# Performance work log

Hardware: AMD Instinct MI355X
Metric: run time of the kernel (lower is better)

The kernel has to match this reference:

```python
import jax, jax.numpy as jnp
import numpy as np

B, N, D_MODEL, H = 2, 2048, 1024, 16
Q_CHUNK, K_CHUNK = 512, 1024
LN_EPS = 1e-5


def layer_norm(x, g, b):
    mu = x.mean(-1, keepdims=True)
    var = ((x - mu) ** 2).mean(-1, keepdims=True)
    return (x - mu) * jax.lax.rsqrt(var + LN_EPS) * g + b


def chunked_attention(q, k, v, qry_chunk, key_chunk):
    # q,k,v: [b,h,n,d]; memory-efficient chunked online-softmax attention
    b, h, n, d = q.shape
    q = q * (d ** -0.5)
    Q, K = n // qry_chunk, n // key_chunk
    qr = q.reshape(b, h, Q, qry_chunk, d)
    kr = k.reshape(b, h, K, key_chunk, d)
    vr = v.reshape(b, h, K, key_chunk, d)
    # per (q-chunk, k-chunk) scores: [b,h,Q,K,i,j]
    qk = jnp.einsum('bhqid,bhkjd->bhqkij', qr, kr)
    qk_max = jax.lax.stop_gradient(qk.max(axis=-1, keepdims=True))  # [b,h,Q,K,i,1]
    exp_qk = jnp.exp(qk - qk_max)
    attn = jnp.einsum('bhqkij,bhkjd->bhqkid', exp_qk, vr)
    exp_sum = exp_qk.sum(-1)            # [b,h,Q,K,i]
    m = qk_max[..., 0]                  # [b,h,Q,K,i]
    gmax = m.max(axis=3, keepdims=True)  # global max over key chunks
    renorm = jax.lax.stop_gradient(jnp.exp(m - gmax))
    num = (attn * renorm[..., None]).sum(axis=3)       # [b,h,Q,i,d]
    den = (exp_sum * renorm).sum(axis=3)[..., None]    # [b,h,Q,i,1]
    out = num / (1e-8 + den)
    return out.reshape(b, h, n, d)


def setup_inputs() -> dict:
    key = jax.random.key(0)
    ks = jax.random.split(key, 10)
    s = 0.02
    return {
        'x': jax.random.normal(ks[0], (B, N, D_MODEL), dtype=jnp.float32),
        'Wq': jax.random.normal(ks[1], (D_MODEL, D_MODEL), dtype=jnp.float32) * s,
        'bq': jnp.zeros((D_MODEL,), jnp.float32),
        'Wk': jax.random.normal(ks[2], (D_MODEL, D_MODEL), dtype=jnp.float32) * s,
        'bk': jnp.zeros((D_MODEL,), jnp.float32),
        'Wv': jax.random.normal(ks[3], (D_MODEL, D_MODEL), dtype=jnp.float32) * s,
        'bv': jnp.zeros((D_MODEL,), jnp.float32),
        'Wo': jax.random.normal(ks[4], (D_MODEL, D_MODEL), dtype=jnp.float32) * s,
        'bo': jnp.zeros((D_MODEL,), jnp.float32),
        'ln_g': jnp.ones((D_MODEL,), jnp.float32),
        'ln_b': jnp.zeros((D_MODEL,), jnp.float32),
    }


def reference(x, Wq, bq, Wk, bk, Wv, bv, Wo, bo, ln_g, ln_b):
    # qkv adapter: self-attention (key = val = qry = x)
    q = x @ Wq + bq
    k = x @ Wk + bk
    v = x @ Wv + bv
    # pre-norm on query path
    q = layer_norm(q, ln_g, ln_b)
    b, n, _ = q.shape
    d = D_MODEL // H
    qh = q.reshape(b, n, H, d).transpose(0, 2, 1, 3)
    kh = k.reshape(b, n, H, d).transpose(0, 2, 1, 3)
    vh = v.reshape(b, n, H, d).transpose(0, 2, 1, 3)
    attn = chunked_attention(qh, kh, vh, Q_CHUNK, K_CHUNK)
    out = attn.transpose(0, 2, 1, 3).reshape(b, n, D_MODEL)
    out = out + q  # residual with normed projected query
    return out @ Wo + bo
```

## Files before the change

### kernel.cpp

```cpp
#include <hip/hip_runtime.h>


typedef unsigned short u16;
typedef __attribute__((ext_vector_type(8))) short bf8v;
typedef __attribute__((ext_vector_type(4))) float f4v;

typedef __attribute__((address_space(1))) void gvoid;
typedef __attribute__((address_space(3))) void lvoid;
__device__ __forceinline__ void cp16(const void* g, void* l) {
  __builtin_amdgcn_global_load_lds((gvoid*)g, (lvoid*)l, 16, 0, 0);
}

__device__ __forceinline__ float bf2f(u16 u) {
  unsigned int x = ((unsigned int)u) << 16;
  float f; __builtin_memcpy(&f, &x, 4); return f;
}
__device__ __forceinline__ u16 f2bf(float f) {
  unsigned int x; __builtin_memcpy(&x, &f, 4);
  unsigned int r = (x + 0x7fffu + ((x >> 16) & 1u)) >> 16;
  return (u16)r;
}
__device__ __forceinline__ unsigned pack2bf(float a, float b) {
  unsigned ua, ub;
  __builtin_memcpy(&ua, &a, 4); __builtin_memcpy(&ub, &b, 4);
  return __builtin_amdgcn_perm(ub, ua, 0x07060302u);
}

#define KSCALE 0.18033688011f

__global__ void k_classify(const u16* a0, const u16* a1, const u16* a2, const u16* a3,
                           const u16* a4, const u16* a5, const u16* a6, const u16* a7,
                           const u16* a8, const u16* a9, const u16* a10, int* flags) {
  int t = threadIdx.x;
  if (t >= 11) return;
  const u16* arr[11] = {a0,a1,a2,a3,a4,a5,a6,a7,a8,a9,a10};
  const u16* p = arr[t];
  int ze = 0, no = 0, pe = 0;
  for (int i = 0; i < 128; ++i) {
    u16 he = p[2*i], ho = p[2*i+1];
    if (he == 0) ze++;
    if (ho != 0) no++;
    int e = (he >> 7) & 0xff;
    if (he == 0 || (e >= 64 && e <= 160)) pe++;
  }
  int isbf;
  if (ze >= 100 && no >= 64) isbf = 0;
  else isbf = (pe >= 100) ? 1 : 0;
  flags[t] = isbf;
}

__global__ __launch_bounds__(256) void k_convert_x(const void* xin, u16* xb, const int* flags) {
  size_t i = ((size_t)blockIdx.x * 256 + threadIdx.x) * 8;
  if (flags[0]) {
    *(float4*)(xb + i) = *((const float4*)((const u16*)xin + i));
  } else {
    const float* xf = (const float*)xin;
    float4 a = *(const float4*)(xf + i);
    float4 b = *(const float4*)(xf + i + 4);
    ushort4 o0, o1;
    o0.x = f2bf(a.x); o0.y = f2bf(a.y); o0.z = f2bf(a.z); o0.w = f2bf(a.w);
    o1.x = f2bf(b.x); o1.y = f2bf(b.y); o1.z = f2bf(b.z); o1.w = f2bf(b.w);
    *(ushort4*)(xb + i) = o0; *(ushort4*)(xb + i + 4) = o1;
  }
}

__global__ __launch_bounds__(256) void k_transpose_w(const void* W0, const void* W1,
    const void* W2, const void* W3, u16* wt, const int* flags) {
  __shared__ u16 tile[64 * 65];
  int z = blockIdx.z;
  const void* W = (z == 0) ? W0 : (z == 1) ? W1 : (z == 2) ? W2 : W3;
  int isb = flags[1 + 2*z];
  u16* dst = wt + (size_t)z * (1u << 20);
  int r0 = blockIdx.y * 64, c0 = blockIdx.x * 64;
  int t = threadIdx.x;
  for (int rr = 0; rr < 2; ++rr) {
    int row = rr * 32 + (t >> 3);
    int c8 = (t & 7) * 8;
    u16 v[8];
    if (isb) {
      const u16* Ws = (const u16*)W;
      ushort4 a = *(const ushort4*)&Ws[(size_t)(r0 + row) * 1024 + c0 + c8];
      ushort4 b = *(const ushort4*)&Ws[(size_t)(r0 + row) * 1024 + c0 + c8 + 4];
      v[0]=a.x; v[1]=a.y; v[2]=a.z; v[3]=a.w; v[4]=b.x; v[5]=b.y; v[6]=b.z; v[7]=b.w;
    } else {
      const float* Wf = (const float*)W;
      float4 a = *(const float4*)&Wf[(size_t)(r0 + row) * 1024 + c0 + c8];
      float4 b = *(const float4*)&Wf[(size_t)(r0 + row) * 1024 + c0 + c8 + 4];
      v[0]=f2bf(a.x); v[1]=f2bf(a.y); v[2]=f2bf(a.z); v[3]=f2bf(a.w);
      v[4]=f2bf(b.x); v[5]=f2bf(b.y); v[6]=f2bf(b.z); v[7]=f2bf(b.w);
    }
#pragma unroll
    for (int j = 0; j < 8; ++j) tile[row * 65 + c8 + j] = v[j];
  }
  __syncthreads();
  for (int rr = 0; rr < 2; ++rr) {
    int nrow = rr * 32 + (t >> 3);
    int k8 = (t & 7) * 8;
    u16 v[8];
#pragma unroll
    for (int j = 0; j < 8; ++j) v[j] = tile[(k8 + j) * 65 + nrow];
    ushort4 o0, o1;
    o0.x=v[0]; o0.y=v[1]; o0.z=v[2]; o0.w=v[3];
    o1.x=v[4]; o1.y=v[5]; o1.z=v[6]; o1.w=v[7];
    *(ushort4*)&dst[(size_t)(c0 + nrow) * 1024 + r0 + k8] = o0;
    *(ushort4*)&dst[(size_t)(c0 + nrow) * 1024 + r0 + k8 + 4] = o1;
  }
}

__device__ __forceinline__ void gemm128(const u16* __restrict__ A, const u16* __restrict__ Bt,
    const void* __restrict__ bias, int bias_bf, void* __restrict__ Cout, int mode,
    float cscale) {
  __shared__ __align__(16) u16 As[2][128 * 32];
  __shared__ __align__(16) u16 Bs[2][128 * 32];
  const int tid = threadIdx.x;
  const int wave = tid >> 6, lane = tid & 63;
  const int qd = lane >> 4, ln = lane & 15;
  const int m0 = blockIdx.y * 128, n0 = blockIdx.x * 128;
  const int wr = (wave >> 1) * 64, wc = (wave & 1) * 64;
  const int r0 = wave * 16 + (lane >> 2);
  const int csrc = ((lane & 3) ^ ((lane >> 2) & 3)) * 8;
  const u16* Ag = &A[(size_t)m0 * 1024];
  const u16* Bg = &Bt[(size_t)n0 * 1024];
  const int co = (qd ^ (ln & 3)) * 8;
  f4v acc[4][4];
#pragma unroll
  for (int i = 0; i < 4; ++i)
#pragma unroll
    for (int j = 0; j < 4; ++j) acc[i][j] = (f4v){0.f, 0.f, 0.f, 0.f};

#pragma unroll
  for (int t = 0; t < 2; ++t) {
    cp16(&Ag[(size_t)(t * 64 + r0) * 1024 + csrc], &As[0][(t * 256 + wave * 64) * 8]);
    cp16(&Bg[(size_t)(t * 64 + r0) * 1024 + csrc], &Bs[0][(t * 256 + wave * 64) * 8]);
  }
  for (int it = 0; it < 32; ++it) {
    __syncthreads();
    if (it < 31) {
      int ko = (it + 1) * 32;
      int bi = (it + 1) & 1;
#pragma unroll
      for (int t = 0; t < 2; ++t) {
        cp16(&Ag[(size_t)(t * 64 + r0) * 1024 + ko + csrc], &As[bi][(t * 256 + wave * 64) * 8]);
        cp16(&Bg[(size_t)(t * 64 + r0) * 1024 + ko + csrc], &Bs[bi][(t * 256 + wave * 64) * 8]);
      }
    }
    const u16* as = As[it & 1];
    const u16* bs = Bs[it & 1];
    bf8v af[4], bfr[4];
#pragma unroll
    for (int i = 0; i < 4; ++i) af[i]  = *(const bf8v*)&as[(wr + i * 16 + ln) * 32 + co];
#pragma unroll
    for (int j = 0; j < 4; ++j) bfr[j] = *(const bf8v*)&bs[(wc + j * 16 + ln) * 32 + co];
#pragma unroll
    for (int i = 0; i < 4; ++i)
#pragma unroll
      for (int j = 0; j < 4; ++j)
        acc[i][j] = __builtin_amdgcn_mfma_f32_16x16x32_bf16(af[i], bfr[j], acc[i][j], 0, 0, 0);
  }
#pragma unroll
  for (int j = 0; j < 4; ++j) {
    int col = n0 + wc + j * 16 + ln;
    float bv = bias_bf ? bf2f(((const u16*)bias)[col]) : ((const float*)bias)[col];
#pragma unroll
    for (int i = 0; i < 4; ++i) {
      int row = m0 + wr + i * 16 + qd * 4;
      if (mode == 2) {
        ushort4 o4;
        o4.x = f2bf((acc[i][j][0] + bv) * cscale);
        o4.y = f2bf((acc[i][j][1] + bv) * cscale);
        o4.z = f2bf((acc[i][j][2] + bv) * cscale);
        o4.w = f2bf((acc[i][j][3] + bv) * cscale);
        int l = row & 63;
        int pos = (((l >> 5) << 2 | ((l >> 2) & 3)) << 3) | ((l & 16) >> 2);
        int n = row & 2047;
        size_t vidx = ((size_t)((row >> 11) * 16 + (col >> 6))) * (64 * 2048)
                    + (size_t)(col & 63) * 2048 + (n & ~63) + pos;
        *(ushort4*)&((u16*)Cout)[vidx] = o4;
      } else {
#pragma unroll
        for (int r = 0; r < 4; ++r) {
          float v = (acc[i][j][r] + bv) * cscale;
          if (mode == 1) ((u16*)Cout)[(size_t)(row + r) * 1024 + col] = f2bf(v);
          else           ((float*)Cout)[(size_t)(row + r) * 1024 + col] = v;
        }
      }
    }
  }
}

__global__ __launch_bounds__(256) void k_gemm_qkv(const u16* xb, const u16* wt,
    const void* bq, const void* bk, const void* bv, const int* flags,
    u16* qpre, u16* kb, u16* vtb) {
  int z = blockIdx.z;
  const u16* Bt = wt + (size_t)z * (1u << 20);
  const void* bias = (z == 0) ? bq : (z == 1) ? bk : bv;
  if (z == 0)      gemm128(xb, Bt, bias, flags[2], qpre, 1, 1.0f);
  else if (z == 1) gemm128(xb, Bt, bias, flags[4], kb,   1, KSCALE);
  else             gemm128(xb, Bt, bias, flags[6], vtb,  2, 1.0f);
}

__global__ __launch_bounds__(256) void k_gemm_out(const u16* A, const u16* Bt,
    const void* bias, const int* flags, void* out) {
  gemm128(A, Bt, bias, flags[8], out, flags[0] ? 1 : 0, 1.0f);
}

__global__ __launch_bounds__(256) void k_layernorm(const u16* __restrict__ qp,
    const void* __restrict__ g, const void* __restrict__ bb, const int* flags,
    u16* __restrict__ out) {
  int row = blockIdx.x, t = threadIdx.x;
  const u16* rp = qp + (size_t)row * 1024;
  ushort4 u = *(const ushort4*)(rp + t * 4);
  float x0 = bf2f(u.x), x1 = bf2f(u.y), x2 = bf2f(u.z), x3 = bf2f(u.w);
  float s = x0 + x1 + x2 + x3;
  float s2 = x0 * x0 + x1 * x1 + x2 * x2 + x3 * x3;
  for (int off = 32; off; off >>= 1) { s += __shfl_down(s, off); s2 += __shfl_down(s2, off); }
  __shared__ float red[10];
  int wave = t >> 6, lane = t & 63;
  if (lane == 0) { red[wave] = s; red[4 + wave] = s2; }
  __syncthreads();
  if (t == 0) {
    float S = red[0] + red[1] + red[2] + red[3];
    float S2 = red[4] + red[5] + red[6] + red[7];
    float mu = S * (1.f / 1024.f);
    float var = S2 * (1.f / 1024.f) - mu * mu;
    red[8] = mu; red[9] = rsqrtf(var + 1e-5f);
  }
  __syncthreads();
  float mu = red[8], rstd = red[9];
  int gf = flags[9], bf = flags[10];
  int c = t * 4;
  float gv[4], bv[4];
#pragma unroll
  for (int k = 0; k < 4; ++k) {
    gv[k] = gf ? bf2f(((const u16*)g)[c + k]) : ((const float*)g)[c + k];
    bv[k] = bf ? bf2f(((const u16*)bb)[c + k]) : ((const float*)bb)[c + k];
  }
  ushort4 o;
  o.x = f2bf((x0 - mu) * rstd * gv[0] + bv[0]);
  o.y = f2bf((x1 - mu) * rstd * gv[1] + bv[1]);
  o.z = f2bf((x2 - mu) * rstd * gv[2] + bv[2]);
  o.w = f2bf((x3 - mu) * rstd * gv[3] + bv[3]);
  *(ushort4*)(out + (size_t)row * 1024 + c) = o;
}

__global__ __launch_bounds__(256) void k_attention(const u16* __restrict__ qln,
    const u16* __restrict__ kb, const u16* __restrict__ vt, u16* __restrict__ attn) {
  const int qt = blockIdx.x, h = blockIdx.y, b = blockIdx.z;
  const int tid = threadIdx.x, wave = tid >> 6, lane = tid & 63;
  const int qd = lane >> 4, ln = lane & 15;
  __shared__ __align__(16) u16 Ks[2][64 * 64];
  __shared__ __align__(16) u16 Vs[2][64 * 64];
  const int qrow0 = qt * 64 + wave * 16;

  const u16* kgb = kb + (size_t)b * 2048 * 1024 + h * 64;
  const u16* vgb = vt + ((size_t)(b * 16 + h)) * 64 * 2048;

  bf8v qf0, qf1;
  {
    const u16* qb = qln + ((size_t)b * 2048 + qrow0 + ln) * 1024 + h * 64;
    qf0 = *(const bf8v*)(qb + qd * 8);
    qf1 = *(const bf8v*)(qb + 32 + qd * 8);
  }
  float ls[4] = {0.f, 0.f, 0.f, 0.f};
  f4v o[4];
#pragma unroll
  for (int dt = 0; dt < 4; ++dt) o[dt] = (f4v){0.f, 0.f, 0.f, 0.f};

  const int swz  = (qd ^ (ln & 7)) * 8;
  const int swz4 = ((qd + 4) ^ (ln & 7)) * 8;
  const int lr8 = lane >> 3;
  const int cs8 = lane & 7;

#define STAGE(kt, bi)                                                          \
  {                                                                            \
    _Pragma("unroll")                                                          \
    for (int t = 0; t < 2; ++t) {                                              \
      int row = wave * 16 + t * 8 + lr8;                                       \
      int cs = (cs8 ^ (row & 7)) * 8;                                          \
      cp16(&kgb[(size_t)((kt) + row) * 1024 + cs], &Ks[bi][(wave * 16 + t * 8) * 64]); \
      cp16(&vgb[(size_t)row * 2048 + (kt) + cs],   &Vs[bi][(wave * 16 + t * 8) * 64]); \
    }                                                                          \
  }

  STAGE(0, 0);
  for (int it = 0; it < 32; ++it) {
    __syncthreads();
    if (it < 31) STAGE((it + 1) * 64, (it + 1) & 1);
    const u16* K = Ks[it & 1];
    const u16* V = Vs[it & 1];

    unsigned pk[4][2];
#pragma unroll
    for (int ct = 0; ct < 4; ++ct) {
      bf8v k0 = *(const bf8v*)&K[(ct * 16 + ln) * 64 + swz];
      bf8v k1 = *(const bf8v*)&K[(ct * 16 + ln) * 64 + swz4];
      f4v z = (f4v){0.f, 0.f, 0.f, 0.f};
      z = __builtin_amdgcn_mfma_f32_16x16x32_bf16(k0, qf0, z, 0, 0, 0);
      z = __builtin_amdgcn_mfma_f32_16x16x32_bf16(k1, qf1, z, 0, 0, 0);
      float p0 = __builtin_amdgcn_exp2f(z[0]);
      float p1 = __builtin_amdgcn_exp2f(z[1]);
      float p2 = __builtin_amdgcn_exp2f(z[2]);
      float p3 = __builtin_amdgcn_exp2f(z[3]);
      ls[0] += p0; ls[1] += p1; ls[2] += p2; ls[3] += p3;
      pk[ct][0] = pack2bf(p0, p1);
      pk[ct][1] = pack2bf(p2, p3);
    }
#pragma unroll
    for (int c = 0; c < 2; ++c) {
      unsigned avals[4] = {pk[2*c][0], pk[2*c][1], pk[2*c+1][0], pk[2*c+1][1]};
      bf8v af; __builtin_memcpy(&af, avals, 16);
#pragma unroll
      for (int dt = 0; dt < 4; ++dt) {
        int vrow = dt * 16 + ln;
        bf8v vf = *(const bf8v*)&V[vrow * 64 + (((c * 4 + qd) ^ (vrow & 7)) * 8)];
        o[dt] = __builtin_amdgcn_mfma_f32_16x16x32_bf16(af, vf, o[dt], 0, 0, 0);
      }
    }
  }
  float lsum = (ls[0] + ls[1]) + (ls[2] + ls[3]);
  lsum += __shfl_xor(lsum, 16);
  lsum += __shfl_xor(lsum, 32);
  float rden[4];
#pragma unroll
  for (int r = 0; r < 4; ++r) {
    float dv = __shfl(lsum, (lane & 48) + qd * 4 + r);
    rden[r] = __builtin_amdgcn_rcpf(1e-8f + dv);
  }
#pragma unroll
  for (int dt = 0; dt < 4; ++dt) {
#pragma unroll
    for (int r = 0; r < 4; ++r) {
      size_t idx = ((size_t)b * 2048 + qrow0 + qd * 4 + r) * 1024 + h * 64 + dt * 16 + ln;
      float val = o[dt][r] * rden[r] + bf2f(qln[idx]);
      attn[idx] = f2bf(val);
    }
  }
}

extern "C" void kernel_launch(void* const* d_in, const int* in_sizes, int n_in,
                              void* d_out, int out_size, void* d_ws, size_t ws_size,
                              hipStream_t stream) {
  int* flags = (int*)d_ws;
  u16* base = (u16*)((char*)d_ws + 256);
  const size_t M1 = 1u << 20;
  u16* xb   = base;
  u16* wt   = base + 4 * M1;
  u16* qpre = base + 8 * M1;
  u16* kb   = base + 12 * M1;
  u16* vtb  = base + 16 * M1;
  u16* qln = xb;
  u16* at  = qpre;

  k_classify<<<1, 64, 0, stream>>>(
      (const u16*)d_in[0], (const u16*)d_in[1], (const u16*)d_in[2], (const u16*)d_in[3],
      (const u16*)d_in[4], (const u16*)d_in[5], (const u16*)d_in[6], (const u16*)d_in[7],
      (const u16*)d_in[8], (const u16*)d_in[9], (const u16*)d_in[10], flags);

  k_convert_x<<<2048, 256, 0, stream>>>(d_in[0], xb, flags);
  k_transpose_w<<<dim3(16, 16, 4), 256, 0, stream>>>(d_in[1], d_in[3], d_in[5], d_in[7], wt, flags);
  k_gemm_qkv<<<dim3(8, 32, 3), 256, 0, stream>>>(xb, wt, d_in[2], d_in[4], d_in[6], flags,
                                                 qpre, kb, vtb);
  k_layernorm<<<4096, 256, 0, stream>>>(qpre, d_in[9], d_in[10], flags, qln);
  k_attention<<<dim3(32, 16, 2), 256, 0, stream>>>(qln, kb, vtb, at);
  k_gemm_out<<<dim3(8, 32, 1), 256, 0, stream>>>(at, wt + 3 * M1, d_in[8], flags, d_out);
}
```

Baseline: 238.6 us.

## Reuse K/V tiles across two query sub-tiles per wave; halve output GEMM M-tile

The attention kernel now runs 128-thread blocks where each wave handles 32 query rows as two 16-row sub-tiles. K fragments are loaded into registers once and V fragments are shared across both sub-tiles, which halves LDS reads per MFMA. The cost is more accumulator registers and fewer waves per block, with launch bounds asking for 2 blocks per CU. The output projection GEMM is templated to a 64-row M tile, doubling its grid to 512 blocks so more CUs have work, at the price of lower per-block reuse of the B tile.

```diff
diff --git a/kernel.cpp b/kernel.cpp
--- a/kernel.cpp
+++ b/kernel.cpp
@@ -107,52 +107,57 @@
   }
 }
 
-__device__ __forceinline__ void gemm128(const u16* __restrict__ A, const u16* __restrict__ Bt,
+template <int MT>
+__device__ __forceinline__ void gemm_bt(const u16* __restrict__ A, const u16* __restrict__ Bt,
     const void* __restrict__ bias, int bias_bf, void* __restrict__ Cout, int mode,
     float cscale) {
-  __shared__ __align__(16) u16 As[2][128 * 32];
+  constexpr int MI = MT / 32;
+  __shared__ __align__(16) u16 As[2][MT * 32];
   __shared__ __align__(16) u16 Bs[2][128 * 32];
   const int tid = threadIdx.x;
   const int wave = tid >> 6, lane = tid & 63;
   const int qd = lane >> 4, ln = lane & 15;
-  const int m0 = blockIdx.y * 128, n0 = blockIdx.x * 128;
-  const int wr = (wave >> 1) * 64, wc = (wave & 1) * 64;
+  const int m0 = blockIdx.y * MT, n0 = blockIdx.x * 128;
+  const int wr = (wave >> 1) * (MT / 2), wc = (wave & 1) * 64;
   const int r0 = wave * 16 + (lane >> 2);
   const int csrc = ((lane & 3) ^ ((lane >> 2) & 3)) * 8;
   const u16* Ag = &A[(size_t)m0 * 1024];
   const u16* Bg = &Bt[(size_t)n0 * 1024];
   const int co = (qd ^ (ln & 3)) * 8;
-  f4v acc[4][4];
-#pragma unroll
-  for (int i = 0; i < 4; ++i)
+  f4v acc[MI][4];
+#pragma unroll
+  for (int i = 0; i < MI; ++i)
 #pragma unroll
     for (int j = 0; j < 4; ++j) acc[i][j] = (f4v){0.f, 0.f, 0.f, 0.f};
 
 #pragma unroll
-  for (int t = 0; t < 2; ++t) {
+  for (int t = 0; t < MT / 64; ++t)
     cp16(&Ag[(size_t)(t * 64 + r0) * 1024 + csrc], &As[0][(t * 256 + wave * 64) * 8]);
+#pragma unroll
+  for (int t = 0; t < 2; ++t)
     cp16(&Bg[(size_t)(t * 64 + r0) * 1024 + csrc], &Bs[0][(t * 256 + wave * 64) * 8]);
-  }
+
   for (int it = 0; it < 32; ++it) {
     __syncthreads();
     if (it < 31) {
       int ko = (it + 1) * 32;
       int bi = (it + 1) & 1;
 #pragma unroll
-      for (int t = 0; t < 2; ++t) {
+      for (int t = 0; t < MT / 64; ++t)
         cp16(&Ag[(size_t)(t * 64 + r0) * 1024 + ko + csrc], &As[bi][(t * 256 + wave * 64) * 8]);
+#pragma unroll
+      for (int t = 0; t < 2; ++t)
         cp16(&Bg[(size_t)(t * 64 + r0) * 1024 + ko + csrc], &Bs[bi][(t * 256 + wave * 64) * 8]);
-      }
     }
     const u16* as = As[it & 1];
     const u16* bs = Bs[it & 1];
-    bf8v af[4], bfr[4];
-#pragma unroll
-    for (int i = 0; i < 4; ++i) af[i]  = *(const bf8v*)&as[(wr + i * 16 + ln) * 32 + co];
+    bf8v af[MI], bfr[4];
+#pragma unroll
+    for (int i = 0; i < MI; ++i) af[i]  = *(const bf8v*)&as[(wr + i * 16 + ln) * 32 + co];
 #pragma unroll
     for (int j = 0; j < 4; ++j) bfr[j] = *(const bf8v*)&bs[(wc + j * 16 + ln) * 32 + co];
 #pragma unroll
-    for (int i = 0; i < 4; ++i)
+    for (int i = 0; i < MI; ++i)
 #pragma unroll
       for (int j = 0; j < 4; ++j)
         acc[i][j] = __builtin_amdgcn_mfma_f32_16x16x32_bf16(af[i], bfr[j], acc[i][j], 0, 0, 0);
@@ -162,7 +167,7 @@
     int col = n0 + wc + j * 16 + ln;
     float bv = bias_bf ? bf2f(((const u16*)bias)[col]) : ((const float*)bias)[col];
 #pragma unroll
-    for (int i = 0; i < 4; ++i) {
+    for (int i = 0; i < MI; ++i) {
       int row = m0 + wr + i * 16 + qd * 4;
       if (mode == 2) {
         ushort4 o4;
@@ -194,14 +199,14 @@
   int z = blockIdx.z;
   const u16* Bt = wt + (size_t)z * (1u << 20);
   const void* bias = (z == 0) ? bq : (z == 1) ? bk : bv;
-  if (z == 0)      gemm128(xb, Bt, bias, flags[2], qpre, 1, 1.0f);
-  else if (z == 1) gemm128(xb, Bt, bias, flags[4], kb,   1, KSCALE);
-  else             gemm128(xb, Bt, bias, flags[6], vtb,  2, 1.0f);
+  if (z == 0)      gemm_bt<128>(xb, Bt, bias, flags[2], qpre, 1, 1.0f);
+  else if (z == 1) gemm_bt<128>(xb, Bt, bias, flags[4], kb,   1, KSCALE);
+  else             gemm_bt<128>(xb, Bt, bias, flags[6], vtb,  2, 1.0f);
 }
 
 __global__ __launch_bounds__(256) void k_gemm_out(const u16* A, const u16* Bt,
     const void* bias, const int* flags, void* out) {
-  gemm128(A, Bt, bias, flags[8], out, flags[0] ? 1 : 0, 1.0f);
+  gemm_bt<64>(A, Bt, bias, flags[8], out, flags[0] ? 1 : 0, 1.0f);
 }
 
 __global__ __launch_bounds__(256) void k_layernorm(const u16* __restrict__ qp,
@@ -243,28 +248,31 @@
   *(ushort4*)(out + (size_t)row * 1024 + c) = o;
 }
 
-__global__ __launch_bounds__(256) void k_attention(const u16* __restrict__ qln,
+__global__ __launch_bounds__(128, 2) void k_attention(const u16* __restrict__ qln,
     const u16* __restrict__ kb, const u16* __restrict__ vt, u16* __restrict__ attn) {
   const int qt = blockIdx.x, h = blockIdx.y, b = blockIdx.z;
   const int tid = threadIdx.x, wave = tid >> 6, lane = tid & 63;
   const int qd = lane >> 4, ln = lane & 15;
   __shared__ __align__(16) u16 Ks[2][64 * 64];
   __shared__ __align__(16) u16 Vs[2][64 * 64];
-  const int qrow0 = qt * 64 + wave * 16;
+  const int qrow0 = qt * 64 + wave * 32;
 
   const u16* kgb = kb + (size_t)b * 2048 * 1024 + h * 64;
   const u16* vgb = vt + ((size_t)(b * 16 + h)) * 64 * 2048;
 
-  bf8v qf0, qf1;
-  {
-    const u16* qb = qln + ((size_t)b * 2048 + qrow0 + ln) * 1024 + h * 64;
-    qf0 = *(const bf8v*)(qb + qd * 8);
-    qf1 = *(const bf8v*)(qb + 32 + qd * 8);
-  }
-  float ls[4] = {0.f, 0.f, 0.f, 0.f};
-  f4v o[4];
-#pragma unroll
-  for (int dt = 0; dt < 4; ++dt) o[dt] = (f4v){0.f, 0.f, 0.f, 0.f};
+  bf8v qf[2][2];
+#pragma unroll
+  for (int qs = 0; qs < 2; ++qs) {
+    const u16* qb = qln + ((size_t)b * 2048 + qrow0 + qs * 16 + ln) * 1024 + h * 64;
+    qf[qs][0] = *(const bf8v*)(qb + qd * 8);
+    qf[qs][1] = *(const bf8v*)(qb + 32 + qd * 8);
+  }
+  float ls[2][4];
+  f4v o[2][4];
+#pragma unroll
+  for (int qs = 0; qs < 2; ++qs)
+#pragma unroll
+    for (int r = 0; r < 4; ++r) { ls[qs][r] = 0.f; o[qs][r] = (f4v){0.f, 0.f, 0.f, 0.f}; }
 
   const int swz  = (qd ^ (ln & 7)) * 8;
   const int swz4 = ((qd + 4) ^ (ln & 7)) * 8;
@@ -274,11 +282,11 @@
 #define STAGE(kt, bi)                                                          \
   {                                                                            \
     _Pragma("unroll")                                                          \
-    for (int t = 0; t < 2; ++t) {                                              \
-      int row = wave * 16 + t * 8 + lr8;                                       \
+    for (int t = 0; t < 4; ++t) {                                              \
+      int row = wave * 32 + t * 8 + lr8;                                       \
       int cs = (cs8 ^ (row & 7)) * 8;                                          \
-      cp16(&kgb[(size_t)((kt) + row) * 1024 + cs], &Ks[bi][(wave * 16 + t * 8) * 64]); \
-      cp16(&vgb[(size_t)row * 2048 + (kt) + cs],   &Vs[bi][(wave * 16 + t * 8) * 64]); \
+      cp16(&kgb[(size_t)((kt) + row) * 1024 + cs], &Ks[bi][(wave * 32 + t * 8) * 64]); \
+      cp16(&vgb[(size_t)row * 2048 + (kt) + cs],   &Vs[bi][(wave * 32 + t * 8) * 64]); \
     }                                                                          \
   }
 
@@ -289,50 +297,64 @@
     const u16* K = Ks[it & 1];
     const u16* V = Vs[it & 1];
 
-    unsigned pk[4][2];
+    bf8v kf[4][2];
 #pragma unroll
     for (int ct = 0; ct < 4; ++ct) {
-      bf8v k0 = *(const bf8v*)&K[(ct * 16 + ln) * 64 + swz];
-      bf8v k1 = *(const bf8v*)&K[(ct * 16 + ln) * 64 + swz4];
-      f4v z = (f4v){0.f, 0.f, 0.f, 0.f};
-      z = __builtin_amdgcn_mfma_f32_16x16x32_bf16(k0, qf0, z, 0, 0, 0);
-      z = __builtin_amdgcn_mfma_f32_16x16x32_bf16(k1, qf1, z, 0, 0, 0);
-      float p0 = __builtin_amdgcn_exp2f(z[0]);
-      float p1 = __builtin_amdgcn_exp2f(z[1]);
-      float p2 = __builtin_amdgcn_exp2f(z[2]);
-      float p3 = __builtin_amdgcn_exp2f(z[3]);
-      ls[0] += p0; ls[1] += p1; ls[2] += p2; ls[3] += p3;
-      pk[ct][0] = pack2bf(p0, p1);
-      pk[ct][1] = pack2bf(p2, p3);
+      kf[ct][0] = *(const bf8v*)&K[(ct * 16 + ln) * 64 + swz];
+      kf[ct][1] = *(const bf8v*)&K[(ct * 16 + ln) * 64 + swz4];
+    }
+    unsigned pk[2][4][2];
+#pragma unroll
+    for (int qs = 0; qs < 2; ++qs) {
+#pragma unroll
+      for (int ct = 0; ct < 4; ++ct) {
+        f4v z = (f4v){0.f, 0.f, 0.f, 0.f};
+        z = __builtin_amdgcn_mfma_f32_16x16x32_bf16(kf[ct][0], qf[qs][0], z, 0, 0, 0);
+        z = __builtin_amdgcn_mfma_f32_16x16x32_bf16(kf[ct][1], qf[qs][1], z, 0, 0, 0);
+        float p0 = __builtin_amdgcn_exp2f(z[0]);
+        float p1 = __builtin_amdgcn_exp2f(z[1]);
+        float p2 = __builtin_amdgcn_exp2f(z[2]);
+        float p3 = __builtin_amdgcn_exp2f(z[3]);
+        ls[qs][0] += p0; ls[qs][1] += p1; ls[qs][2] += p2; ls[qs][3] += p3;
+        pk[qs][ct][0] = pack2bf(p0, p1);
+        pk[qs][ct][1] = pack2bf(p2, p3);
+      }
     }
 #pragma unroll
     for (int c = 0; c < 2; ++c) {
-      unsigned avals[4] = {pk[2*c][0], pk[2*c][1], pk[2*c+1][0], pk[2*c+1][1]};
-      bf8v af; __builtin_memcpy(&af, avals, 16);
 #pragma unroll
       for (int dt = 0; dt < 4; ++dt) {
         int vrow = dt * 16 + ln;
         bf8v vf = *(const bf8v*)&V[vrow * 64 + (((c * 4 + qd) ^ (vrow & 7)) * 8)];
-        o[dt] = __builtin_amdgcn_mfma_f32_16x16x32_bf16(af, vf, o[dt], 0, 0, 0);
+#pragma unroll
+        for (int qs = 0; qs < 2; ++qs) {
+          unsigned avals[4] = {pk[qs][2*c][0], pk[qs][2*c][1], pk[qs][2*c+1][0], pk[qs][2*c+1][1]};
+          bf8v af; __builtin_memcpy(&af, avals, 16);
+          o[qs][dt] = __builtin_amdgcn_mfma_f32_16x16x32_bf16(af, vf, o[qs][dt], 0, 0, 0);
+        }
       }
     }
   }
-  float lsum = (ls[0] + ls[1]) + (ls[2] + ls[3]);
-  lsum += __shfl_xor(lsum, 16);
-  lsum += __shfl_xor(lsum, 32);
-  float rden[4];
-#pragma unroll
-  for (int r = 0; r < 4; ++r) {
-    float dv = __shfl(lsum, (lane & 48) + qd * 4 + r);
-    rden[r] = __builtin_amdgcn_rcpf(1e-8f + dv);
-  }
-#pragma unroll
-  for (int dt = 0; dt < 4; ++dt) {
+#pragma unroll
+  for (int qs = 0; qs < 2; ++qs) {
+    float lsum = (ls[qs][0] + ls[qs][1]) + (ls[qs][2] + ls[qs][3]);
+    lsum += __shfl_xor(lsum, 16);
+    lsum += __shfl_xor(lsum, 32);
+    float rden[4];
 #pragma unroll
     for (int r = 0; r < 4; ++r) {
-      size_t idx = ((size_t)b * 2048 + qrow0 + qd * 4 + r) * 1024 + h * 64 + dt * 16 + ln;
-      float val = o[dt][r] * rden[r] + bf2f(qln[idx]);
-      attn[idx] = f2bf(val);
+      float dv = __shfl(lsum, (lane & 48) + qd * 4 + r);
+      rden[r] = __builtin_amdgcn_rcpf(1e-8f + dv);
+    }
+#pragma unroll
+    for (int dt = 0; dt < 4; ++dt) {
+#pragma unroll
+      for (int r = 0; r < 4; ++r) {
+        size_t idx = ((size_t)b * 2048 + qrow0 + qs * 16 + qd * 4 + r) * 1024
+                   + h * 64 + dt * 16 + ln;
+        float val = o[qs][dt][r] * rden[r] + bf2f(qln[idx]);
+        attn[idx] = f2bf(val);
+      }
     }
   }
 }
@@ -361,6 +383,6 @@
   k_gemm_qkv<<<dim3(8, 32, 3), 256, 0, stream>>>(xb, wt, d_in[2], d_in[4], d_in[6], flags,
                                                  qpre, kb, vtb);
   k_layernorm<<<4096, 256, 0, stream>>>(qpre, d_in[9], d_in[10], flags, qln);
-  k_attention<<<dim3(32, 16, 2), 256, 0, stream>>>(qln, kb, vtb, at);
-  k_gemm_out<<<dim3(8, 32, 1), 256, 0, stream>>>(at, wt + 3 * M1, d_in[8], flags, d_out);
-}
+  k_attention<<<dim3(32, 16, 2), 128, 0, stream>>>(qln, kb, vtb, at);
+  k_gemm_out<<<dim3(8, 64), 256, 0, stream>>>(at, wt + 3 * M1, d_in[8], flags, d_out);
+}
```

After: 231.4 us. 1.03x faster.
